# Performance work log

Hardware: AMD Instinct MI355X
Metric: run time of the kernel (lower is better)

Reference implementation:

```python
import jax, jax.numpy as jnp
import numpy as np

NUM_GROUPS = 32
EPS = 1e-5
HT_MIN = -1.0
HT_MAX = 1.0


def setup_inputs() -> dict:
    key = jax.random.key(0)
    k1, k2, k3 = jax.random.split(key, 3)
    B, IN, OUT = 8192, 2048, 4096
    x = jax.random.normal(k1, (B, IN), dtype=jnp.float32)
    # kaiming-uniform-ish scale for weight, uniform bias in [-1/sqrt(fan_in), 1/sqrt(fan_in)]
    bound_w = np.sqrt(1.0 / IN)
    weight = jax.random.uniform(k2, (OUT, IN), dtype=jnp.float32, minval=-bound_w, maxval=bound_w)
    bias = jax.random.uniform(k3, (OUT,), dtype=jnp.float32, minval=-bound_w, maxval=bound_w)
    return {"x": x, "weight": weight, "bias": bias}


def reference(x, weight, bias):
    # GEMM + bias: (B, out)
    y = jnp.einsum('bi,oi->bo', x, weight) + bias
    B, OUT = y.shape
    fpg = OUT // NUM_GROUPS
    g = y.reshape(B, NUM_GROUPS, fpg)
    mean = jnp.mean(g, axis=-1, keepdims=True)
    var = jnp.mean(jnp.square(g - mean), axis=-1, keepdims=True)  # biased variance
    x_hat = (g - mean) / jnp.sqrt(var + EPS)
    out = jnp.clip(x_hat, HT_MIN, HT_MAX)
    return out.reshape(B, OUT)
```

## Files before the change

kernel.cpp:

```cpp
#include <hip/hip_runtime.h>
#include <hip/hip_bf16.h>

#define B_ROWS   8192
#define K_DIM    2048
#define OUT_COLS 4096
#define EPS      1e-5f

#define BM 256
#define BN 256
#define BK 64
#define NT (K_DIM / BK)

using f32x4  = __attribute__((ext_vector_type(4))) float;
using bf16x8 = __attribute__((ext_vector_type(8))) short;

__device__ __forceinline__ unsigned short f2bf_rn(float f) {
    unsigned u = __builtin_bit_cast(unsigned, f);
    u += 0x7FFFu + ((u >> 16) & 1u);
    return (unsigned short)(u >> 16);
}

__global__ void cvt_all(const float* __restrict__ x, const float* __restrict__ w,
                        unsigned short* __restrict__ xb, unsigned short* __restrict__ wb) {
    const int n4x = (B_ROWS * K_DIM) / 4;
    const int n4w = (OUT_COLS * K_DIM) / 4;
    int stride = gridDim.x * blockDim.x;
    for (int i = blockIdx.x * blockDim.x + threadIdx.x; i < n4x + n4w; i += stride) {
        const float4* src; ushort4* dst; int j;
        if (i < n4x) { src = (const float4*)x; dst = (ushort4*)xb; j = i; }
        else         { src = (const float4*)w; dst = (ushort4*)wb; j = i - n4x; }
        float4 v = src[j];
        ushort4 r;
        r.x = f2bf_rn(v.x); r.y = f2bf_rn(v.y); r.z = f2bf_rn(v.z); r.w = f2bf_rn(v.w);
        dst[j] = r;
    }
}

__device__ __forceinline__ void gload16(const unsigned short* src, unsigned short* lds) {
    __builtin_amdgcn_global_load_lds((const __attribute__((address_space(1))) void*)src,
                                     (__attribute__((address_space(3))) void*)lds,
                                     16, 0, 0);
}

__device__ __forceinline__ float rowsum16(float v) {
    int x;
    x = __builtin_amdgcn_update_dpp(0, __builtin_bit_cast(int, v), 0x121, 0xF, 0xF, true);
    v += __builtin_bit_cast(float, x);
    x = __builtin_amdgcn_update_dpp(0, __builtin_bit_cast(int, v), 0x122, 0xF, 0xF, true);
    v += __builtin_bit_cast(float, x);
    x = __builtin_amdgcn_update_dpp(0, __builtin_bit_cast(int, v), 0x124, 0xF, 0xF, true);
    v += __builtin_bit_cast(float, x);
    x = __builtin_amdgcn_update_dpp(0, __builtin_bit_cast(int, v), 0x128, 0xF, 0xF, true);
    v += __builtin_bit_cast(float, x);
    return v;
}

#define STA(BUF, H, KT) do {                                                        \
    gload16(Ag + (H)*262144 + (KT)*64 + goff0, &As[BUF][(H)*8192 + lds0]);          \
    gload16(Ag + (H)*262144 + (KT)*64 + goff1, &As[BUF][(H)*8192 + lds1]);          \
  } while (0)
#define STB(BUF, H, KT) do {                                                        \
    gload16(Bg + (H)*262144 + (KT)*64 + goff0, &Bs[BUF][(H)*8192 + lds0]);          \
    gload16(Bg + (H)*262144 + (KT)*64 + goff1, &Bs[BUF][(H)*8192 + lds1]);          \
  } while (0)

#define RD_B(CURB) do {                                                             \
    _Pragma("unroll") for (int n = 0; n < 4; ++n) {                                 \
      const int ro = browb + n * 16 * BK;                                           \
      bb[n][0] = *(const bf16x8*)&(CURB)[ro + colsw0];                              \
      bb[n][1] = *(const bf16x8*)&(CURB)[ro + colsw1];                              \
    } } while (0)

#define RD_A(SLOT, CURA, Q) do {                                                    \
    _Pragma("unroll") for (int dm = 0; dm < 2; ++dm) {                              \
      const int ro = arow + (2*(Q)+dm) * 16 * BK;                                   \
      af[SLOT][dm][0] = *(const bf16x8*)&(CURA)[ro + colsw0];                       \
      af[SLOT][dm][1] = *(const bf16x8*)&(CURA)[ro + colsw1];                       \
    } } while (0)

#define MFMA16(SLOT, Q) do {                                                        \
    __builtin_amdgcn_s_setprio(1);                                                  \
    _Pragma("unroll") for (int kk = 0; kk < 2; ++kk)                                \
      _Pragma("unroll") for (int dm = 0; dm < 2; ++dm)                              \
        _Pragma("unroll") for (int n = 0; n < 4; ++n)                               \
          acc[2*(Q)+dm][n] = __builtin_amdgcn_mfma_f32_16x16x32_bf16(               \
              af[SLOT][dm][kk], bb[n][kk], acc[2*(Q)+dm][n], 0, 0, 0);              \
    __builtin_amdgcn_s_setprio(0);                                                  \
  } while (0)

#define VW4  asm volatile("s_waitcnt vmcnt(4)" ::: "memory")
#define BAR  __builtin_amdgcn_s_barrier()

__global__ __launch_bounds__(512, 2) void gemm_gn(const unsigned short* __restrict__ A,
                                                  const unsigned short* __restrict__ Bw,
                                                  const float* __restrict__ bias,
                                                  float* __restrict__ out) {
    __shared__ __align__(16) unsigned short As[2][16384];
    __shared__ __align__(16) unsigned short Bs[2][16384];
    __shared__ __align__(16) float redbuf[256 * 8];

    const int tid  = threadIdx.x;
    const int lane = tid & 63;
    const int wave = tid >> 6;
    const int wr   = wave >> 2;
    const int wcn  = wave & 3;
    const int l16  = lane & 15;
    const int lhi  = lane >> 4;

    const int bid  = blockIdx.x;
    const int swz  = (bid & 7) * (gridDim.x >> 3) + (bid >> 3);
    const int brow = swz >> 4;
    const int bcol = swz & 15;

    int goff0, goff1, lds0, lds1;
    {
        int f0 = tid;          int r0 = f0 >> 3;
        int f1 = 512 + tid;    int r1 = f1 >> 3;
        goff0 = r0 * K_DIM + (((f0 & 7) ^ (r0 & 7)) * 8);
        goff1 = r1 * K_DIM + (((f1 & 7) ^ (r1 & 7)) * 8);
        lds0  = f0 * 8;
        lds1  = f1 * 8;
    }
    const unsigned short* Ag = A  + (size_t)brow * BM * K_DIM;
    const unsigned short* Bg = Bw + (size_t)bcol * BN * K_DIM;

    const int colsw0 = (0 * 32 + lhi * 8) ^ ((l16 & 7) << 3);
    const int colsw1 = (1 * 32 + lhi * 8) ^ ((l16 & 7) << 3);
    const int arow   = (wr * 128 + l16) * BK;
    const int browb  = (wcn * 64 + l16) * BK;

    const unsigned short* A0p = &As[0][0];
    const unsigned short* A1p = &As[1][0];
    const unsigned short* B0p = &Bs[0][0];
    const unsigned short* B1p = &Bs[1][0];

    f32x4  acc[8][4];
    {
        float bv[4];
        #pragma unroll
        for (int n = 0; n < 4; ++n)
            bv[n] = bias[bcol * BN + wcn * 64 + n * 16 + l16];
        #pragma unroll
        for (int m = 0; m < 8; ++m)
            #pragma unroll
            for (int n = 0; n < 4; ++n)
                #pragma unroll
                for (int j = 0; j < 4; ++j)
                    acc[m][n][j] = bv[n];
    }

    bf16x8 af[2][2][2];
    bf16x8 bb[4][2];

    STA(0, 0, 0); STA(0, 1, 0);
    STB(0, 0, 0); STB(0, 1, 0);
    STB(1, 0, 1); STB(1, 1, 1);
    VW4;
    BAR;
    RD_A(0, A0p, 0);
    RD_B(B0p);

    #pragma unroll 1
    for (int tt = 0; tt < NT; tt += 2) {
        const int k1 = (tt + 1) & (NT - 1);
        const int k2 = (tt + 2) & (NT - 1);
        const int k3 = (tt + 3) & (NT - 1);
        RD_A(1, A0p, 1); STA(1, 0, k1);               MFMA16(0, 0);       BAR;
        RD_A(0, A0p, 2); STA(1, 1, k1); STB(0, 0, k2); MFMA16(1, 1);      BAR;
        RD_A(1, A0p, 3); STB(0, 1, k2);               MFMA16(0, 2); VW4;  BAR;
        RD_A(0, A1p, 0);                              MFMA16(1, 3); RD_B(B1p); BAR;
        RD_A(1, A1p, 1); STA(0, 0, k2);               MFMA16(0, 0);       BAR;
        RD_A(0, A1p, 2); STA(0, 1, k2); STB(1, 0, k3); MFMA16(1, 1);      BAR;
        RD_A(1, A1p, 3); STB(1, 1, k3);               MFMA16(0, 2); VW4;  BAR;
        RD_A(0, A0p, 0);                              MFMA16(1, 3); RD_B(B0p); BAR;
    }

    #pragma unroll
    for (int m = 0; m < 8; ++m) {
        #pragma unroll
        for (int j = 0; j < 4; ++j) {
            float s = 0.f, s2 = 0.f;
            #pragma unroll
            for (int n = 0; n < 4; ++n) {
                float v = acc[m][n][j];
                s += v; s2 += v * v;
            }
            s  = rowsum16(s);
            s2 = rowsum16(s2);
            if (l16 == 0) {
                int r = wr * 128 + m * 16 + lhi * 4 + j;
                redbuf[r * 8 + wcn * 2 + 0] = s;
                redbuf[r * 8 + wcn * 2 + 1] = s2;
            }
        }
    }
    asm volatile("s_waitcnt vmcnt(0)" ::: "memory");
    __syncthreads();

    const int p2 = (wcn & 2) * 2;
    #pragma unroll
    for (int m = 0; m < 8; ++m) {
        #pragma unroll
        for (int j = 0; j < 4; ++j) {
            const int r = wr * 128 + m * 16 + lhi * 4 + j;
            const float4 q = *(const float4*)&redbuf[r * 8 + p2];
            const float mean = (q.x + q.z) * (1.0f / 128.0f);
            const float var  = (q.y + q.w) * (1.0f / 128.0f) - mean * mean;
            const float rstd = rsqrtf(var + EPS);
            float* orow = out + (size_t)(brow * BM + r) * OUT_COLS + bcol * BN + wcn * 64 + l16;
            #pragma unroll
            for (int n = 0; n < 4; ++n) {
                float v = (acc[m][n][j] - mean) * rstd;
                v = fminf(fmaxf(v, -1.0f), 1.0f);
                orow[n * 16] = v;
            }
        }
    }
}

extern "C" void kernel_launch(void* const* d_in, const int* in_sizes, int n_in,
                              void* d_out, int out_size, void* d_ws, size_t ws_size,
                              hipStream_t stream) {
    const float* x    = (const float*)d_in[0];
    const float* w    = (const float*)d_in[1];
    const float* bias = (const float*)d_in[2];
    float* out        = (float*)d_out;

    unsigned short* xb = (unsigned short*)d_ws;
    unsigned short* wb = xb + (size_t)B_ROWS * K_DIM;

    cvt_all<<<3072, 256, 0, stream>>>(x, w, xb, wb);

    dim3 grid((B_ROWS / BM) * (OUT_COLS / BN));
    gemm_gn<<<grid, 512, 0, stream>>>(xb, wb, bias, out);
}
```

Before: 157.9 us.

## Restructure GEMM main loop into barrier-fenced phases with double-buffered B fragments

Rewrites the K-loop schedule into eight explicit phases. Each phase issues LDS reads and global-to-LDS stages, then hits a barrier, waits on lgkmcnt(0) and a sched_barrier, and runs its MFMA block at raised priority. The A fragment register double-buffer is dropped so A is read just before use. B fragments are now double-buffered (bbA/bbB), and the next B tile is loaded in halves during the earlier phases. The aim is to make the LDS/MFMA interleave deterministic and to reduce compiler-induced stalls. In exchange, LDS read latency is exposed before each MFMA group, and the new phases add an extra barrier each.

```diff
diff --git a/kernel.cpp b/kernel.cpp
--- a/kernel.cpp
+++ b/kernel.cpp
@@ -64,32 +64,43 @@
     gload16(Bg + (H)*262144 + (KT)*64 + goff1, &Bs[BUF][(H)*8192 + lds1]);          \
   } while (0)
 
-#define RD_B(CURB) do {                                                             \
+#define RD_BH(DST, CURB, KK) do {                                                   \
     _Pragma("unroll") for (int n = 0; n < 4; ++n) {                                 \
       const int ro = browb + n * 16 * BK;                                           \
-      bb[n][0] = *(const bf16x8*)&(CURB)[ro + colsw0];                              \
-      bb[n][1] = *(const bf16x8*)&(CURB)[ro + colsw1];                              \
+      DST[n][KK] = *(const bf16x8*)&(CURB)[ro + ((KK) ? colsw1 : colsw0)];          \
     } } while (0)
 
-#define RD_A(SLOT, CURA, Q) do {                                                    \
+#define RD_A(CURA, Q) do {                                                          \
     _Pragma("unroll") for (int dm = 0; dm < 2; ++dm) {                              \
       const int ro = arow + (2*(Q)+dm) * 16 * BK;                                   \
-      af[SLOT][dm][0] = *(const bf16x8*)&(CURA)[ro + colsw0];                       \
-      af[SLOT][dm][1] = *(const bf16x8*)&(CURA)[ro + colsw1];                       \
+      af[dm][0] = *(const bf16x8*)&(CURA)[ro + colsw0];                             \
+      af[dm][1] = *(const bf16x8*)&(CURA)[ro + colsw1];                             \
     } } while (0)
 
-#define MFMA16(SLOT, Q) do {                                                        \
-    __builtin_amdgcn_s_setprio(1);                                                  \
+#define MFMAQ(BB, Q) do {                                                           \
     _Pragma("unroll") for (int kk = 0; kk < 2; ++kk)                                \
       _Pragma("unroll") for (int dm = 0; dm < 2; ++dm)                              \
         _Pragma("unroll") for (int n = 0; n < 4; ++n)                               \
           acc[2*(Q)+dm][n] = __builtin_amdgcn_mfma_f32_16x16x32_bf16(               \
-              af[SLOT][dm][kk], bb[n][kk], acc[2*(Q)+dm][n], 0, 0, 0);              \
-    __builtin_amdgcn_s_setprio(0);                                                  \
+              af[dm][kk], BB[n][kk], acc[2*(Q)+dm][n], 0, 0, 0);                    \
   } while (0)
 
 #define VW4  asm volatile("s_waitcnt vmcnt(4)" ::: "memory")
 #define BAR  __builtin_amdgcn_s_barrier()
+
+#define PH(PRERD, STAGE, MFMAS, TAILW) do {                                         \
+    PRERD; STAGE;                                                                   \
+    __builtin_amdgcn_s_barrier();                                                   \
+    asm volatile("s_waitcnt lgkmcnt(0)" ::: "memory");                              \
+    __builtin_amdgcn_sched_barrier(0);                                              \
+    __builtin_amdgcn_s_setprio(1);                                                  \
+    MFMAS;                                                                          \
+    __builtin_amdgcn_s_setprio(0);                                                  \
+    TAILW;                                                                          \
+    __builtin_amdgcn_s_barrier();                                                   \
+  } while (0)
+
+#define NOP_ ((void)0)
 
 __global__ __launch_bounds__(512, 2) void gemm_gn(const unsigned short* __restrict__ A,
                                                   const unsigned short* __restrict__ Bw,
@@ -134,7 +145,7 @@
     const unsigned short* B0p = &Bs[0][0];
     const unsigned short* B1p = &Bs[1][0];
 
-    f32x4  acc[8][4];
+    f32x4 acc[8][4];
     {
         float bv[4];
         #pragma unroll
@@ -149,30 +160,30 @@
                     acc[m][n][j] = bv[n];
     }
 
-    bf16x8 af[2][2][2];
-    bf16x8 bb[4][2];
+    bf16x8 af[2][2];
+    bf16x8 bbA[4][2];
+    bf16x8 bbB[4][2];
 
     STA(0, 0, 0); STA(0, 1, 0);
     STB(0, 0, 0); STB(0, 1, 0);
     STB(1, 0, 1); STB(1, 1, 1);
     VW4;
     BAR;
-    RD_A(0, A0p, 0);
-    RD_B(B0p);
+    RD_BH(bbA, B0p, 0); RD_BH(bbA, B0p, 1);
 
     #pragma unroll 1
     for (int tt = 0; tt < NT; tt += 2) {
         const int k1 = (tt + 1) & (NT - 1);
         const int k2 = (tt + 2) & (NT - 1);
         const int k3 = (tt + 3) & (NT - 1);
-        RD_A(1, A0p, 1); STA(1, 0, k1);               MFMA16(0, 0);       BAR;
-        RD_A(0, A0p, 2); STA(1, 1, k1); STB(0, 0, k2); MFMA16(1, 1);      BAR;
-        RD_A(1, A0p, 3); STB(0, 1, k2);               MFMA16(0, 2); VW4;  BAR;
-        RD_A(0, A1p, 0);                              MFMA16(1, 3); RD_B(B1p); BAR;
-        RD_A(1, A1p, 1); STA(0, 0, k2);               MFMA16(0, 0);       BAR;
-        RD_A(0, A1p, 2); STA(0, 1, k2); STB(1, 0, k3); MFMA16(1, 1);      BAR;
-        RD_A(1, A1p, 3); STB(1, 1, k3);               MFMA16(0, 2); VW4;  BAR;
-        RD_A(0, A0p, 0);                              MFMA16(1, 3); RD_B(B0p); BAR;
+        PH( RD_A(A0p, 0),                     STA(1,0,k1); STA(1,1,k1),  MFMAQ(bbA, 0), NOP_ );
+        PH( RD_A(A0p, 1),                     STB(0,0,k2); STB(0,1,k2),  MFMAQ(bbA, 1), VW4  );
+        PH( RD_A(A0p, 2); RD_BH(bbB, B1p, 0), NOP_,                      MFMAQ(bbA, 2), NOP_ );
+        PH( RD_A(A0p, 3); RD_BH(bbB, B1p, 1), NOP_,                      MFMAQ(bbA, 3), NOP_ );
+        PH( RD_A(A1p, 0),                     STA(0,0,k2); STA(0,1,k2),  MFMAQ(bbB, 0), NOP_ );
+        PH( RD_A(A1p, 1),                     STB(1,0,k3); STB(1,1,k3),  MFMAQ(bbB, 1), VW4  );
+        PH( RD_A(A1p, 2); RD_BH(bbA, B0p, 0), NOP_,                      MFMAQ(bbB, 2), NOP_ );
+        PH( RD_A(A1p, 3); RD_BH(bbA, B0p, 1), NOP_,                      MFMAQ(bbB, 3), NOP_ );
     }
 
     #pragma unroll
```

New measurement: 170.5 us. +8.0%, slower.

## Shrink GEMM tile to 128x256x32 with triple-buffered LDS pipeline

Applied to the files above, without the earlier changes.

Reduces the block tile from 256x256 with BK=64 to 128x256 with BK=32. The double-buffered, eight-phase loop is replaced by a three-stage LDS ring where each k-tile issues the next prefetch, reads fragments, runs 16 MFMAs and then waits and barriers. With half the accumulators and less LDS, launch bounds ask for 4 blocks per CU to raise occupancy and hide latency. The costs are lower arithmetic intensity per block, more global reloads of the weight tile, and a barrier on every small k-step.

```diff
diff --git a/kernel.cpp b/kernel.cpp
--- a/kernel.cpp
+++ b/kernel.cpp
@@ -6,10 +6,10 @@
 #define OUT_COLS 4096
 #define EPS      1e-5f
 
-#define BM 256
+#define BM 128
 #define BN 256
-#define BK 64
-#define NT (K_DIM / BK)
+#define BK 32
+#define NKT (K_DIM / BK)
 
 using f32x4  = __attribute__((ext_vector_type(4))) float;
 using bf16x8 = __attribute__((ext_vector_type(8))) short;
@@ -55,49 +55,40 @@
     return v;
 }
 
-#define STA(BUF, H, KT) do {                                                        \
-    gload16(Ag + (H)*262144 + (KT)*64 + goff0, &As[BUF][(H)*8192 + lds0]);          \
-    gload16(Ag + (H)*262144 + (KT)*64 + goff1, &As[BUF][(H)*8192 + lds1]);          \
+#define VW3   asm volatile("s_waitcnt vmcnt(3)" ::: "memory")
+#define VWALL asm volatile("s_waitcnt vmcnt(0)" ::: "memory")
+#define BAR   __builtin_amdgcn_s_barrier()
+
+#define STAGE(AOFF, BOFF, KT) do {                                                  \
+    gload16(Ag + (KT)*32 + goffA,  &As[(AOFF) + ldsA]);                             \
+    gload16(Bg + (KT)*32 + goffB0, &Bs[(BOFF) + ldsB0]);                            \
+    gload16(Bg + (KT)*32 + goffB1, &Bs[(BOFF) + ldsB1]);                            \
   } while (0)
-#define STB(BUF, H, KT) do {                                                        \
-    gload16(Bg + (H)*262144 + (KT)*64 + goff0, &Bs[BUF][(H)*8192 + lds0]);          \
-    gload16(Bg + (H)*262144 + (KT)*64 + goff1, &Bs[BUF][(H)*8192 + lds1]);          \
+
+#define KTILE(AOFF, BOFF, SAOFF, SBOFF, KT2) do {                                   \
+    bf16x8 af[4], bb[4];                                                            \
+    STAGE(SAOFF, SBOFF, KT2);                                                       \
+    _Pragma("unroll") for (int m = 0; m < 4; ++m)                                   \
+        af[m] = *(const bf16x8*)&As[(AOFF) + arow + m*512 + csw];                   \
+    _Pragma("unroll") for (int n = 0; n < 4; ++n)                                   \
+        bb[n] = *(const bf16x8*)&Bs[(BOFF) + brw + n*512 + csw];                    \
+    __builtin_amdgcn_s_setprio(1);                                                  \
+    _Pragma("unroll") for (int m = 0; m < 4; ++m)                                   \
+      _Pragma("unroll") for (int n = 0; n < 4; ++n)                                 \
+        acc[m][n] = __builtin_amdgcn_mfma_f32_16x16x32_bf16(                        \
+            af[m], bb[n], acc[m][n], 0, 0, 0);                                      \
+    __builtin_amdgcn_s_setprio(0);                                                  \
+    VW3;                                                                            \
+    BAR;                                                                            \
   } while (0)
 
-#define RD_B(CURB) do {                                                             \
-    _Pragma("unroll") for (int n = 0; n < 4; ++n) {                                 \
-      const int ro = browb + n * 16 * BK;                                           \
-      bb[n][0] = *(const bf16x8*)&(CURB)[ro + colsw0];                              \
-      bb[n][1] = *(const bf16x8*)&(CURB)[ro + colsw1];                              \
-    } } while (0)
-
-#define RD_A(SLOT, CURA, Q) do {                                                    \
-    _Pragma("unroll") for (int dm = 0; dm < 2; ++dm) {                              \
-      const int ro = arow + (2*(Q)+dm) * 16 * BK;                                   \
-      af[SLOT][dm][0] = *(const bf16x8*)&(CURA)[ro + colsw0];                       \
-      af[SLOT][dm][1] = *(const bf16x8*)&(CURA)[ro + colsw1];                       \
-    } } while (0)
-
-#define MFMA16(SLOT, Q) do {                                                        \
-    __builtin_amdgcn_s_setprio(1);                                                  \
-    _Pragma("unroll") for (int kk = 0; kk < 2; ++kk)                                \
-      _Pragma("unroll") for (int dm = 0; dm < 2; ++dm)                              \
-        _Pragma("unroll") for (int n = 0; n < 4; ++n)                               \
-          acc[2*(Q)+dm][n] = __builtin_amdgcn_mfma_f32_16x16x32_bf16(               \
-              af[SLOT][dm][kk], bb[n][kk], acc[2*(Q)+dm][n], 0, 0, 0);              \
-    __builtin_amdgcn_s_setprio(0);                                                  \
-  } while (0)
-
-#define VW4  asm volatile("s_waitcnt vmcnt(4)" ::: "memory")
-#define BAR  __builtin_amdgcn_s_barrier()
-
-__global__ __launch_bounds__(512, 2) void gemm_gn(const unsigned short* __restrict__ A,
+__global__ __launch_bounds__(512, 4) void gemm_gn(const unsigned short* __restrict__ A,
                                                   const unsigned short* __restrict__ Bw,
                                                   const float* __restrict__ bias,
                                                   float* __restrict__ out) {
-    __shared__ __align__(16) unsigned short As[2][16384];
-    __shared__ __align__(16) unsigned short Bs[2][16384];
-    __shared__ __align__(16) float redbuf[256 * 8];
+    __shared__ __align__(16) unsigned short As[3 * 4096];
+    __shared__ __align__(16) unsigned short Bs[3 * 8192];
+    __shared__ __align__(16) float redbuf[128 * 8];
 
     const int tid  = threadIdx.x;
     const int lane = tid & 63;
@@ -112,36 +103,33 @@
     const int brow = swz >> 4;
     const int bcol = swz & 15;
 
-    int goff0, goff1, lds0, lds1;
+    int goffA, ldsA, goffB0, goffB1, ldsB0, ldsB1;
     {
-        int f0 = tid;          int r0 = f0 >> 3;
-        int f1 = 512 + tid;    int r1 = f1 >> 3;
-        goff0 = r0 * K_DIM + (((f0 & 7) ^ (r0 & 7)) * 8);
-        goff1 = r1 * K_DIM + (((f1 & 7) ^ (r1 & 7)) * 8);
-        lds0  = f0 * 8;
-        lds1  = f1 * 8;
+        int sA = tid;              int rA = sA >> 2;
+        goffA  = rA * K_DIM + (((sA & 3) ^ ((rA >> 1) & 3)) * 8);
+        ldsA   = sA * 8;
+        int s0 = tid;              int r0 = s0 >> 2;
+        int s1 = tid + 512;        int r1 = s1 >> 2;
+        goffB0 = r0 * K_DIM + (((s0 & 3) ^ ((r0 >> 1) & 3)) * 8);
+        goffB1 = r1 * K_DIM + (((s1 & 3) ^ ((r1 >> 1) & 3)) * 8);
+        ldsB0  = s0 * 8;
+        ldsB1  = s1 * 8;
     }
     const unsigned short* Ag = A  + (size_t)brow * BM * K_DIM;
     const unsigned short* Bg = Bw + (size_t)bcol * BN * K_DIM;
 
-    const int colsw0 = (0 * 32 + lhi * 8) ^ ((l16 & 7) << 3);
-    const int colsw1 = (1 * 32 + lhi * 8) ^ ((l16 & 7) << 3);
-    const int arow   = (wr * 128 + l16) * BK;
-    const int browb  = (wcn * 64 + l16) * BK;
-
-    const unsigned short* A0p = &As[0][0];
-    const unsigned short* A1p = &As[1][0];
-    const unsigned short* B0p = &Bs[0][0];
-    const unsigned short* B1p = &Bs[1][0];
-
-    f32x4  acc[8][4];
+    const int csw  = (lhi ^ ((l16 >> 1) & 3)) * 8;
+    const int arow = (wr * 64 + l16) * 32;
+    const int brw  = (wcn * 64 + l16) * 32;
+
+    f32x4 acc[4][4];
     {
         float bv[4];
         #pragma unroll
         for (int n = 0; n < 4; ++n)
             bv[n] = bias[bcol * BN + wcn * 64 + n * 16 + l16];
         #pragma unroll
-        for (int m = 0; m < 8; ++m)
+        for (int m = 0; m < 4; ++m)
             #pragma unroll
             for (int n = 0; n < 4; ++n)
                 #pragma unroll
@@ -149,34 +137,36 @@
                     acc[m][n][j] = bv[n];
     }
 
-    bf16x8 af[2][2][2];
-    bf16x8 bb[4][2];
-
-    STA(0, 0, 0); STA(0, 1, 0);
-    STB(0, 0, 0); STB(0, 1, 0);
-    STB(1, 0, 1); STB(1, 1, 1);
-    VW4;
+    STAGE(0, 0, 0);
+    STAGE(4096, 8192, 1);
+    VW3;
     BAR;
-    RD_A(0, A0p, 0);
-    RD_B(B0p);
 
     #pragma unroll 1
-    for (int tt = 0; tt < NT; tt += 2) {
-        const int k1 = (tt + 1) & (NT - 1);
-        const int k2 = (tt + 2) & (NT - 1);
-        const int k3 = (tt + 3) & (NT - 1);
-        RD_A(1, A0p, 1); STA(1, 0, k1);               MFMA16(0, 0);       BAR;
-        RD_A(0, A0p, 2); STA(1, 1, k1); STB(0, 0, k2); MFMA16(1, 1);      BAR;
-        RD_A(1, A0p, 3); STB(0, 1, k2);               MFMA16(0, 2); VW4;  BAR;
-        RD_A(0, A1p, 0);                              MFMA16(1, 3); RD_B(B1p); BAR;
-        RD_A(1, A1p, 1); STA(0, 0, k2);               MFMA16(0, 0);       BAR;
-        RD_A(0, A1p, 2); STA(0, 1, k2); STB(1, 0, k3); MFMA16(1, 1);      BAR;
-        RD_A(1, A1p, 3); STB(1, 1, k3);               MFMA16(0, 2); VW4;  BAR;
-        RD_A(0, A0p, 0);                              MFMA16(1, 3); RD_B(B0p); BAR;
+    for (int it = 0; it < 21; ++it) {
+        const int kt = it * 3;
+        KTILE(0,    0,     8192, 16384, kt + 2);
+        KTILE(4096, 8192,  0,    0,     kt + 3);
+        KTILE(8192, 16384, 4096, 8192,  (kt + 4) & 63);
+    }
+    {
+        bf16x8 af[4], bb[4];
+        #pragma unroll
+        for (int m = 0; m < 4; ++m)
+            af[m] = *(const bf16x8*)&As[arow + m*512 + csw];
+        #pragma unroll
+        for (int n = 0; n < 4; ++n)
+            bb[n] = *(const bf16x8*)&Bs[brw + n*512 + csw];
+        #pragma unroll
+        for (int m = 0; m < 4; ++m)
+            #pragma unroll
+            for (int n = 0; n < 4; ++n)
+                acc[m][n] = __builtin_amdgcn_mfma_f32_16x16x32_bf16(
+                    af[m], bb[n], acc[m][n], 0, 0, 0);
     }
 
     #pragma unroll
-    for (int m = 0; m < 8; ++m) {
+    for (int m = 0; m < 4; ++m) {
         #pragma unroll
         for (int j = 0; j < 4; ++j) {
             float s = 0.f, s2 = 0.f;
@@ -188,21 +178,21 @@
             s  = rowsum16(s);
             s2 = rowsum16(s2);
             if (l16 == 0) {
-                int r = wr * 128 + m * 16 + lhi * 4 + j;
+                int r = wr * 64 + m * 16 + lhi * 4 + j;
                 redbuf[r * 8 + wcn * 2 + 0] = s;
                 redbuf[r * 8 + wcn * 2 + 1] = s2;
             }
         }
     }
-    asm volatile("s_waitcnt vmcnt(0)" ::: "memory");
+    VWALL;
     __syncthreads();
 
     const int p2 = (wcn & 2) * 2;
     #pragma unroll
-    for (int m = 0; m < 8; ++m) {
+    for (int m = 0; m < 4; ++m) {
         #pragma unroll
         for (int j = 0; j < 4; ++j) {
-            const int r = wr * 128 + m * 16 + lhi * 4 + j;
+            const int r = wr * 64 + m * 16 + lhi * 4 + j;
             const float4 q = *(const float4*)&redbuf[r * 8 + p2];
             const float mean = (q.x + q.z) * (1.0f / 128.0f);
             const float var  = (q.y + q.w) * (1.0f / 128.0f) - mean * mean;
```

Measured after the change: 182.1 us. 15.4% more time.
